# Kernel optimization log

Hardware: AMD Instinct MI355X
Metric: run time of the kernel (lower is better)

The kernel has to match this reference:

```python
import jax, jax.numpy as jnp
import numpy as np

EPS = 1e-06
K = 32


def setup_inputs() -> dict:
    key = jax.random.key(0)
    k1, k2, k3, k4, k5 = jax.random.split(key, 5)
    d_model, n_latents = 1024, 16384
    x = jax.random.normal(k1, (2, 2048, d_model), dtype=jnp.float32)
    b_pre = jax.random.normal(k2, (d_model,), dtype=jnp.float32) * 0.02
    W_enc = jax.random.normal(k3, (n_latents, d_model), dtype=jnp.float32) / np.sqrt(d_model)
    b_enc = jax.random.normal(k4, (n_latents,), dtype=jnp.float32) * 0.02
    W_dec = jax.random.normal(k5, (d_model, n_latents), dtype=jnp.float32)
    # mimic normalize_decoder_weights: unit norm along dim=1 (n_latents axis per row)
    W_dec = W_dec / jnp.linalg.norm(W_dec, axis=1, keepdims=True)
    return {"x": x, "b_pre": b_pre, "W_enc": W_enc, "b_enc": b_enc, "W_dec": W_dec}


def reference(x, b_pre, W_enc, b_enc, W_dec):
    B, S, D = x.shape
    # preprocess: center + normalize (torch .std is unbiased, ddof=1)
    mean = jnp.mean(x, axis=-1, keepdims=True)
    norm = jnp.std(x, axis=-1, keepdims=True, ddof=1) + EPS
    xn = ((x - mean) / norm).reshape(-1, D)          # [N, D]
    # encode
    h = (xn - b_pre) @ W_enc.T + b_enc               # [N, n_latents]
    # top-k + relu + scatter into sparse latent
    vals, idx = jax.lax.top_k(h, K)                  # [N, K]
    vals = jax.nn.relu(vals)
    rows = jnp.arange(h.shape[0])[:, None]
    h_sparse = jnp.zeros_like(h).at[rows, idx].set(vals)
    # decode (dense matmul over mostly-zero latents, as in the original)
    recon = h_sparse @ W_dec.T + b_pre               # [N, D]
    # postprocess: denormalize
    recon = recon.reshape(B, S, D) * norm + mean
    return recon
```

## Files before the change

### kernel.cpp

```cpp
#include <hip/hip_runtime.h>
#include <cstdint>
#include <cstddef>

typedef _Float16 half_t;
typedef _Float16 half4_t __attribute__((ext_vector_type(4)));
typedef _Float16 half8_t __attribute__((ext_vector_type(8)));
typedef unsigned short ushort8_t __attribute__((ext_vector_type(8)));
typedef float floatx4 __attribute__((ext_vector_type(4)));

#define NROWS 4096
#define DMODEL 1024
#define NLAT 16384
#define CAND_MAX 256

#define MBYTE (1ull << 20)
static const size_t oW0    = 0;
static const size_t oWdT   = 32 * MBYTE;
static const size_t oMeanF = 64 * MBYTE;
static const size_t oNormF = 64 * MBYTE + (64ull << 10);
static const size_t oMeanD = 64 * MBYTE + (128ull << 10);
static const size_t oNormD = 64 * MBYTE + (192ull << 10);
static const size_t oCandC = 64 * MBYTE + (256ull << 10);
static const size_t oCandI = 65 * MBYTE;
static const size_t oCandV = 69 * MBYTE;
static const size_t oBatch = 77 * MBYTE;

#define BATCH_ROW_BYTES 34816ull

__device__ __forceinline__ void gload16(const void* g, void* l) {
  __builtin_amdgcn_global_load_lds(
      (const __attribute__((address_space(1))) void*)g,
      (__attribute__((address_space(3))) void*)l, 16, 0, 0);
}

__device__ __forceinline__ uint32_t okey16(uint32_t u) {
  return (u & 0x8000u) ? ((~u) & 0xFFFFu) : (u | 0x8000u);
}
__device__ __forceinline__ float inv_okey16(uint32_t k) {
  unsigned short u = (k & 0x8000u) ? (unsigned short)(k & 0x7FFFu)
                                   : (unsigned short)(~k);
  return (float)__builtin_bit_cast(_Float16, u);
}

#define WSPLIT_B 2048
#define TRANS_B  4096
__global__ __launch_bounds__(256) void prepro_kernel(
    const float* __restrict__ x, const float* __restrict__ b_pre,
    const float* __restrict__ W_enc, const float* __restrict__ Wd,
    half_t* __restrict__ W0h, half_t* __restrict__ WdT,
    half_t* __restrict__ X0,
    float* __restrict__ meanF, float* __restrict__ normF,
    double* __restrict__ meanD, double* __restrict__ normD, int r0) {
  int bid = blockIdx.x, tid = threadIdx.x;
  if (bid < WSPLIT_B) {
    size_t base = (size_t)bid * 2048 + tid;
    for (int it = 0; it < 8; ++it) {
      size_t i = base + (size_t)it * 256;
      float4 v = ((const float4*)W_enc)[i];
      half4_t h0;
      h0[0] = (half_t)(v.x * 1024.0f);
      h0[1] = (half_t)(v.y * 1024.0f);
      h0[2] = (half_t)(v.z * 1024.0f);
      h0[3] = (half_t)(v.w * 1024.0f);
      ((half4_t*)W0h)[i] = h0;
    }
    return;
  }
  if (bid < WSPLIT_B + TRANS_B) {
    __shared__ float tile[64][65];
    int t = bid - WSPLIT_B;
    int c0 = (t & 255) * 64;
    int r0t = (t >> 8) * 64;
    int tc = tid & 63, tg = tid >> 6;
    for (int i = 0; i < 16; ++i) {
      int rr = i * 4 + tg;
      tile[rr][tc] = Wd[(size_t)(r0t + rr) * NLAT + c0 + tc];
    }
    __syncthreads();
    for (int i = 0; i < 16; ++i) {
      int cc = i * 4 + tg;
      WdT[(size_t)(c0 + cc) * DMODEL + r0t + tc] = (half_t)tile[tc][cc];
    }
    return;
  }
  int rl = bid - WSPLIT_B - TRANS_B;
  int rg = r0 + rl;
  const float4* px = (const float4*)(x + (size_t)rg * DMODEL);
  float4 v = px[tid];
  double s  = (double)v.x + (double)v.y + (double)v.z + (double)v.w;
  double sq = (double)v.x * v.x + (double)v.y * v.y +
              (double)v.z * v.z + (double)v.w * v.w;
  for (int off = 32; off; off >>= 1) {
    s += __shfl_down(s, off);
    sq += __shfl_down(sq, off);
  }
  __shared__ double ss[4], ssq[4];
  __shared__ double sMean, sNorm;
  int wv = tid >> 6, ln = tid & 63;
  if (ln == 0) { ss[wv] = s; ssq[wv] = sq; }
  __syncthreads();
  if (tid == 0) {
    double S = ss[0] + ss[1] + ss[2] + ss[3];
    double Q = ssq[0] + ssq[1] + ssq[2] + ssq[3];
    double mean = S / (double)DMODEL;
    double var = (Q - (double)DMODEL * mean * mean) / (double)(DMODEL - 1);
    double nrm = sqrt(var) + 1e-6;
    sMean = mean; sNorm = nrm;
    meanF[rg] = (float)mean; normF[rg] = (float)nrm;
    meanD[rg] = mean;        normD[rg] = nrm;
  }
  __syncthreads();
  float mean = (float)sMean, nrm = (float)sNorm;
  const float4* pb = (const float4*)b_pre;
  float4 bp = pb[tid];
  float c[4];
  c[0] = ((v.x - mean) / nrm - bp.x) * 1024.0f;
  c[1] = ((v.y - mean) / nrm - bp.y) * 1024.0f;
  c[2] = ((v.z - mean) / nrm - bp.z) * 1024.0f;
  c[3] = ((v.w - mean) / nrm - bp.w) * 1024.0f;
  half4_t h0;
  for (int i = 0; i < 4; ++i) h0[i] = (half_t)c[i];
  ((half4_t*)(X0 + (size_t)rl * DMODEL))[tid] = h0;
}

__global__ __launch_bounds__(512, 2) void gemm_enc(
    const half_t* __restrict__ X0, const half_t* __restrict__ W0,
    const float* __restrict__ b_enc, half_t* __restrict__ h, int mtiles) {
  __shared__ __align__(16) half_t As[2][256 * 64];
  __shared__ __align__(16) half_t Bs[2][256 * 64];
  int tid = threadIdx.x;
  int lane = tid & 63, wave = tid >> 6;
  int wm = wave >> 2, wn = wave & 3;

  int bid = blockIdx.x;
  int xcd = bid & 7, q = bid >> 3;
  int bn = xcd * 8 + (q & 7);
  int bm = q >> 3;
  (void)mtiles;

  const char* Ag = (const char*)(X0 + (size_t)bm * 256 * DMODEL);
  const char* Bg = (const char*)(W0 + (size_t)bn * 256 * DMODEL);

  int srcSwz = ((lane & 7) ^ (lane >> 3)) << 4;
  int rowBase = wave * 8 + (lane >> 3);
  int ldsWOff = wave * 1024;

#define STAGE(b, kt)                                                          \
  {                                                                           \
    int colB = (kt) * 128 + srcSwz;                                           \
    _Pragma("unroll") for (int i = 0; i < 4; ++i) {                           \
      size_t go = (size_t)(i * 64 + rowBase) * 2048 + colB;                   \
      gload16(Ag + go, (char*)As[b] + i * 8192 + ldsWOff);                    \
      gload16(Bg + go, (char*)Bs[b] + i * 8192 + ldsWOff);                    \
    }                                                                         \
  }

  floatx4 acc[8][4] = {};

  STAGE(0, 0);
  STAGE(1, 1);
  asm volatile("s_waitcnt vmcnt(8)" ::: "memory");
  __builtin_amdgcn_sched_barrier(0);
  __builtin_amdgcn_s_barrier();
  __builtin_amdgcn_sched_barrier(0);

  int laneQ = (lane & 15) * 128 + (lane >> 4) * 16;
  int sxor = (lane & 7) << 4;
  int aRow = wm * 128 * 128;
  int bRow = wn * 64 * 128;

  for (int kt = 0; kt < 16; ++kt) {
    int cur = kt & 1;
    const char* Ab = (const char*)As[cur];
    const char* Bb = (const char*)Bs[cur];
    for (int kk = 0; kk < 2; ++kk) {
      int kOff = kk * 64 + laneQ;
      half8_t a[8], b[4];
#pragma unroll
      for (int mi = 0; mi < 8; ++mi)
        a[mi] = *(const half8_t*)(Ab + ((aRow + mi * 2048 + kOff) ^ sxor));
#pragma unroll
      for (int ni = 0; ni < 4; ++ni)
        b[ni] = *(const half8_t*)(Bb + ((bRow + ni * 2048 + kOff) ^ sxor));
      __builtin_amdgcn_s_setprio(1);
#pragma unroll
      for (int mi = 0; mi < 8; ++mi)
#pragma unroll
        for (int ni = 0; ni < 4; ++ni)
          acc[mi][ni] = __builtin_amdgcn_mfma_f32_16x16x32_f16(
              a[mi], b[ni], acc[mi][ni], 0, 0, 0);
      __builtin_amdgcn_s_setprio(0);
    }
    if (kt == 15) break;
    __builtin_amdgcn_s_barrier();
    if (kt + 2 < 16) {
      STAGE(cur, kt + 2);
      asm volatile("s_waitcnt vmcnt(8)" ::: "memory");
    } else {
      asm volatile("s_waitcnt vmcnt(0)" ::: "memory");
    }
    __builtin_amdgcn_sched_barrier(0);
    __builtin_amdgcn_s_barrier();
    __builtin_amdgcn_sched_barrier(0);
  }
#undef STAGE

  const float scale = 0x1p-20f;
  int rowb = bm * 256 + wm * 128 + ((lane >> 4) * 4);
  int colb = bn * 256 + wn * 64 + (lane & 15);
  float be[4];
#pragma unroll
  for (int ni = 0; ni < 4; ++ni) be[ni] = b_enc[colb + ni * 16];
#pragma unroll
  for (int mi = 0; mi < 8; ++mi)
#pragma unroll
    for (int ni = 0; ni < 4; ++ni)
#pragma unroll
      for (int r = 0; r < 4; ++r)
        h[(size_t)(rowb + mi * 16 + r) * NLAT + colb + ni * 16] =
            (half_t)(acc[mi][ni][r] * scale + be[ni]);
}

__global__ __launch_bounds__(256) void cand_kernel(
    const half_t* __restrict__ h, int* __restrict__ candIdx,
    int* __restrict__ candCnt, int r0) {
  int rl = blockIdx.x, tid = threadIdx.x;
  int rg = r0 + rl;
  const ushort8_t* ph8 = (const ushort8_t*)(h + (size_t)rl * NLAT);
  __shared__ uint32_t hist[8192];
  __shared__ int chunkSum[256];
  __shared__ float sThresh;
  __shared__ int cCount;

  for (int i = tid; i < 8192; i += 256) hist[i] = 0;
  if (tid == 0) cCount = 0;
  __syncthreads();

  for (int i = 0; i < 8; ++i) {
    ushort8_t v = ph8[tid + i * 256];
#pragma unroll
    for (int e = 0; e < 8; ++e)
      atomicAdd(&hist[okey16((uint32_t)v[e]) >> 3], 1u);
  }
  __syncthreads();
  {
    int s = 0;
    for (int b = 0; b < 32; ++b) s += (int)hist[tid * 32 + b];
    chunkSum[tid] = s;
  }
  __syncthreads();
  if (tid == 0) {
    int cum = 0, cchunk = 255;
    for (; cchunk > 0; --cchunk) {
      if (cum + chunkSum[cchunk] >= 32) break;
      cum += chunkSum[cchunk];
    }
    int b = cchunk * 32 + 31;
    for (; b > 0; --b) {
      if (cum + (int)hist[b] >= 32) break;
      cum += (int)hist[b];
    }
    sThresh = inv_okey16((uint32_t)b << 3) - 0.02f;
  }
  __syncthreads();
  float thresh = sThresh;

  for (int i = 0; i < 8; ++i) {
    ushort8_t v = ph8[tid + i * 256];
#pragma unroll
    for (int e = 0; e < 8; ++e) {
      float f = (float)__builtin_bit_cast(_Float16, (unsigned short)v[e]);
      if (f >= thresh) {
        int j = (tid + i * 256) * 8 + e;
        int slot = atomicAdd(&cCount, 1);
        if (slot < CAND_MAX) candIdx[(size_t)rg * CAND_MAX + slot] = j;
      }
    }
  }
  __syncthreads();
  if (tid == 0) candCnt[rg] = (cCount < CAND_MAX) ? cCount : CAND_MAX;
}

__global__ __launch_bounds__(256) void refine_dot(
    const float* __restrict__ x, const float* __restrict__ b_pre,
    const float* __restrict__ W_enc, const float* __restrict__ b_enc,
    const double* __restrict__ meanD, const double* __restrict__ normD,
    const int* __restrict__ candIdx, const int* __restrict__ candCnt,
    double* __restrict__ candV, int r0) {
  int rg = r0 + blockIdx.x;
  int tid = threadIdx.x;
  int wv = tid >> 6, ln = tid & 63;
  double mean = meanD[rg], nrm = normD[rg];
  const float* px = x + (size_t)rg * DMODEL;
  double xr[16];
#pragma unroll
  for (int u = 0; u < 16; ++u)
    xr[u] = ((double)px[ln + u * 64] - mean) / nrm - (double)b_pre[ln + u * 64];
  int nc = candCnt[rg];
  const int* ci = candIdx + (size_t)rg * CAND_MAX;

  for (int c0 = wv * 4; c0 < nc; c0 += 16) {
    const float* wp[4];
#pragma unroll
    for (int q = 0; q < 4; ++q) {
      int c = c0 + q;
      int j = ci[c < nc ? c : (nc - 1)];
      wp[q] = W_enc + (size_t)j * DMODEL + ln;
    }
    double a0 = 0.0, a1 = 0.0, a2 = 0.0, a3 = 0.0;
#pragma unroll
    for (int u = 0; u < 16; ++u) {
      float w0 = wp[0][u * 64];
      float w1 = wp[1][u * 64];
      float w2 = wp[2][u * 64];
      float w3 = wp[3][u * 64];
      a0 += xr[u] * (double)w0;
      a1 += xr[u] * (double)w1;
      a2 += xr[u] * (double)w2;
      a3 += xr[u] * (double)w3;
    }
    double accq[4] = {a0, a1, a2, a3};
#pragma unroll
    for (int q = 0; q < 4; ++q) {
      double s = accq[q];
      for (int off = 32; off; off >>= 1) s += __shfl_down(s, off);
      int c = c0 + q;
      if (ln == 0 && c < nc) {
        int j = ci[c];
        candV[(size_t)rg * CAND_MAX + c] = s + (double)b_enc[j];
      }
    }
  }
}

__global__ __launch_bounds__(256) void sel_decode(
    const double* __restrict__ candV, const int* __restrict__ candIdx,
    const int* __restrict__ candCnt,
    const half_t* __restrict__ WdT, const float* __restrict__ b_pre,
    const float* __restrict__ meanF, const float* __restrict__ normF,
    float* __restrict__ out, int r0) {
  int rg = r0 + blockIdx.x, tid = threadIdx.x;
  __shared__ double cV[CAND_MAX];
  __shared__ int cI[CAND_MAX];
  __shared__ float sVal[32];
  __shared__ int sIdx[32];
  int nc = candCnt[rg];
  for (int c = tid; c < nc; c += 256) {
    cV[c] = candV[(size_t)rg * CAND_MAX + c];
    cI[c] = candIdx[(size_t)rg * CAND_MAX + c];
  }
  if (tid < 32) { sVal[tid] = 0.0f; sIdx[tid] = 0; }
  __syncthreads();
  for (int c = tid; c < nc; c += 256) {
    double v = cV[c];
    int ix = cI[c];
    int rank = 0;
    for (int o = 0; o < nc; ++o) {
      double vo = cV[o];
      int io = cI[o];
      rank += (vo > v || (vo == v && io < ix)) ? 1 : 0;
    }
    if (rank < 32) {
      sIdx[rank] = ix;
      sVal[rank] = (float)(v > 0.0 ? v : 0.0);
    }
  }
  __syncthreads();
  int d0 = tid * 4;
  float4 accv = {0.f, 0.f, 0.f, 0.f};
#pragma unroll 8
  for (int k = 0; k < 32; ++k) {
    float vk = sVal[k];
    const half4_t wv = *(const half4_t*)(WdT + (size_t)sIdx[k] * DMODEL + d0);
    accv.x += vk * (float)wv[0]; accv.y += vk * (float)wv[1];
    accv.z += vk * (float)wv[2]; accv.w += vk * (float)wv[3];
  }
  float4 bp = ((const float4*)b_pre)[tid];
  float nrm = normF[rg], mn = meanF[rg];
  float4 o;
  o.x = (accv.x + bp.x) * nrm + mn;
  o.y = (accv.y + bp.y) * nrm + mn;
  o.z = (accv.z + bp.z) * nrm + mn;
  o.w = (accv.w + bp.w) * nrm + mn;
  ((float4*)(out + (size_t)rg * DMODEL))[tid] = o;
}

extern "C" void kernel_launch(void* const* d_in, const int* in_sizes, int n_in,
                              void* d_out, int out_size, void* d_ws, size_t ws_size,
                              hipStream_t stream) {
  const float* x     = (const float*)d_in[0];
  const float* b_pre = (const float*)d_in[1];
  const float* W_enc = (const float*)d_in[2];
  const float* b_enc = (const float*)d_in[3];
  const float* W_dec = (const float*)d_in[4];
  float* out = (float*)d_out;
  char* ws = (char*)d_ws;

  int rowsB = NROWS;
  while (rowsB > 256) {
    size_t need = oBatch + (size_t)rowsB * BATCH_ROW_BYTES;
    if (need <= ws_size) break;
    rowsB >>= 1;
  }
  if (oBatch + (size_t)rowsB * BATCH_ROW_BYTES > ws_size) return;

  half_t* W0 = (half_t*)(ws + oW0);
  half_t* WdT = (half_t*)(ws + oWdT);
  float* meanF = (float*)(ws + oMeanF);
  float* normF = (float*)(ws + oNormF);
  double* meanD = (double*)(ws + oMeanD);
  double* normD = (double*)(ws + oNormD);
  int*   candCnt = (int*)(ws + oCandC);
  int*   candIdx = (int*)(ws + oCandI);
  double* candV  = (double*)(ws + oCandV);
  half_t* X0b  = (half_t*)(ws + oBatch);
  half_t* hb   = X0b + (size_t)rowsB * DMODEL;

  for (int r0 = 0; r0 < NROWS; r0 += rowsB) {
    hipLaunchKernelGGL(prepro_kernel,
                       dim3(WSPLIT_B + TRANS_B + rowsB), dim3(256), 0, stream,
                       x, b_pre, W_enc, W_dec, W0, WdT, X0b,
                       meanF, normF, meanD, normD, r0);
    int mtiles = rowsB / 256;
    hipLaunchKernelGGL(gemm_enc, dim3(mtiles * 64), dim3(512), 0, stream,
                       X0b, W0, b_enc, hb, mtiles);
    hipLaunchKernelGGL(cand_kernel, dim3(rowsB), dim3(256), 0, stream,
                       hb, candIdx, candCnt, r0);
    hipLaunchKernelGGL(refine_dot, dim3(rowsB), dim3(256), 0, stream,
                       x, b_pre, W_enc, b_enc, meanD, normD, candIdx, candCnt,
                       candV, r0);
    hipLaunchKernelGGL(sel_decode, dim3(rowsB), dim3(256), 0, stream,
                       candV, candIdx, candCnt, WdT, b_pre, meanF, normF, out, r0);
  }
}
```

Before: 378.2 us.

## Interleave staged global loads with MFMA phases in encoder GEMM main loop

Restructures the encoder GEMM K-loop into an 8-phase schedule per pair of tiles. Each phase issues half-tile global-to-LDS loads between fragment reads and MFMA bursts, with barriers and lgkm/vmcnt waits placed explicitly. The goal is to spread memory traffic across compute so load latency hides better than with the old bulk stage-then-compute loop. In exchange there are many more barriers per tile. Loads wrap past the last tile (kt&15), so the final iterations issue redundant loads.

New measurement: 372.7 us. Within noise of the previous version (-1.4%).

```diff
diff --git a/kernel.cpp b/kernel.cpp
--- a/kernel.cpp
+++ b/kernel.cpp
@@ -145,65 +145,93 @@
   int rowBase = wave * 8 + (lane >> 3);
   int ldsWOff = wave * 1024;
 
-#define STAGE(b, kt)                                                          \
-  {                                                                           \
-    int colB = (kt) * 128 + srcSwz;                                           \
-    _Pragma("unroll") for (int i = 0; i < 4; ++i) {                           \
-      size_t go = (size_t)(i * 64 + rowBase) * 2048 + colB;                   \
-      gload16(Ag + go, (char*)As[b] + i * 8192 + ldsWOff);                    \
-      gload16(Bg + go, (char*)Bs[b] + i * 8192 + ldsWOff);                    \
-    }                                                                         \
-  }
+#define STG_A(b, kt, pr) { int colB = ((kt) & 15) * 128 + srcSwz;             \
+    gload16(Ag + (size_t)((pr) * 64 + rowBase) * 2048 + colB,                 \
+            (char*)As[b] + (pr) * 8192 + ldsWOff);                            \
+    gload16(Ag + (size_t)(((pr) + 2) * 64 + rowBase) * 2048 + colB,           \
+            (char*)As[b] + ((pr) + 2) * 8192 + ldsWOff); }
+#define STG_B(b, kt, pr) { int colB = ((kt) & 15) * 128 + srcSwz;             \
+    gload16(Bg + (size_t)((pr) * 64 + rowBase) * 2048 + colB,                 \
+            (char*)Bs[b] + (pr) * 8192 + ldsWOff);                            \
+    gload16(Bg + (size_t)(((pr) + 2) * 64 + rowBase) * 2048 + colB,           \
+            (char*)Bs[b] + ((pr) + 2) * 8192 + ldsWOff); }
 
   floatx4 acc[8][4] = {};
 
-  STAGE(0, 0);
-  STAGE(1, 1);
-  asm volatile("s_waitcnt vmcnt(8)" ::: "memory");
+  STG_B(0, 0, 0); STG_B(0, 0, 1); STG_A(0, 0, 0); STG_A(0, 0, 1);
+  STG_B(1, 1, 0); STG_B(1, 1, 1); STG_A(1, 1, 0);
+  asm volatile("s_waitcnt vmcnt(6)" ::: "memory");
   __builtin_amdgcn_sched_barrier(0);
   __builtin_amdgcn_s_barrier();
-  __builtin_amdgcn_sched_barrier(0);
 
   int laneQ = (lane & 15) * 128 + (lane >> 4) * 16;
   int sxor = (lane & 7) << 4;
   int aRow = wm * 128 * 128;
   int bRow = wn * 64 * 128;
 
-  for (int kt = 0; kt < 16; ++kt) {
-    int cur = kt & 1;
-    const char* Ab = (const char*)As[cur];
-    const char* Bb = (const char*)Bs[cur];
-    for (int kk = 0; kk < 2; ++kk) {
-      int kOff = kk * 64 + laneQ;
-      half8_t a[8], b[4];
-#pragma unroll
-      for (int mi = 0; mi < 8; ++mi)
-        a[mi] = *(const half8_t*)(Ab + ((aRow + mi * 2048 + kOff) ^ sxor));
-#pragma unroll
-      for (int ni = 0; ni < 4; ++ni)
-        b[ni] = *(const half8_t*)(Bb + ((bRow + ni * 2048 + kOff) ^ sxor));
-      __builtin_amdgcn_s_setprio(1);
-#pragma unroll
-      for (int mi = 0; mi < 8; ++mi)
-#pragma unroll
-        for (int ni = 0; ni < 4; ++ni)
-          acc[mi][ni] = __builtin_amdgcn_mfma_f32_16x16x32_f16(
-              a[mi], b[ni], acc[mi][ni], 0, 0, 0);
-      __builtin_amdgcn_s_setprio(0);
-    }
-    if (kt == 15) break;
-    __builtin_amdgcn_s_barrier();
-    if (kt + 2 < 16) {
-      STAGE(cur, kt + 2);
-      asm volatile("s_waitcnt vmcnt(8)" ::: "memory");
-    } else {
-      asm volatile("s_waitcnt vmcnt(0)" ::: "memory");
-    }
-    __builtin_amdgcn_sched_barrier(0);
-    __builtin_amdgcn_s_barrier();
-    __builtin_amdgcn_sched_barrier(0);
-  }
-#undef STAGE
+  half8_t bfr[2][4], afr[4];
+  const char *Ab, *Bb;
+
+#define LD_A(mh, kk) _Pragma("unroll") for (int t = 0; t < 4; ++t)            \
+    afr[t] = *(const half8_t*)(Ab + ((aRow + ((mh) * 4 + t) * 2048 +          \
+                                      (kk) * 64 + laneQ) ^ sxor));
+#define LD_B(kk) _Pragma("unroll") for (int t = 0; t < 4; ++t)                \
+    bfr[kk][t] = *(const half8_t*)(Bb + ((bRow + t * 2048 +                   \
+                                          (kk) * 64 + laneQ) ^ sxor));
+#define MM(mb, kk) __builtin_amdgcn_s_setprio(1);                             \
+    _Pragma("unroll") for (int mi = 0; mi < 4; ++mi)                          \
+    _Pragma("unroll") for (int ni = 0; ni < 4; ++ni)                          \
+      acc[(mb) + mi][ni] = __builtin_amdgcn_mfma_f32_16x16x32_f16(            \
+          afr[mi], bfr[kk][ni], acc[(mb) + mi][ni], 0, 0, 0);                 \
+    __builtin_amdgcn_s_setprio(0);
+#define BAR() __builtin_amdgcn_s_barrier()
+#define LGKM0() { asm volatile("s_waitcnt lgkmcnt(0)" ::: "memory");          \
+    __builtin_amdgcn_sched_barrier(0); }
+#define VM6() { asm volatile("s_waitcnt vmcnt(6)" ::: "memory");              \
+    __builtin_amdgcn_sched_barrier(0); }
+
+#pragma unroll 1
+  for (int i = 0; i < 8; ++i) {
+    int t0 = 2 * i;
+    Ab = (const char*)As[0]; Bb = (const char*)Bs[0];
+    LD_B(0); LD_B(1); LD_A(0, 0);
+    STG_A(1, t0 + 1, 1);
+    BAR(); LGKM0(); MM(0, 0); BAR();
+    LD_A(1, 0);
+    STG_B(0, t0 + 2, 0);
+    BAR(); LGKM0(); MM(4, 0); BAR();
+    LD_A(0, 1);
+    STG_B(0, t0 + 2, 1);
+    BAR(); LGKM0(); MM(0, 1); BAR();
+    LD_A(1, 1);
+    STG_A(0, t0 + 2, 0);
+    BAR(); LGKM0(); MM(4, 1);
+    VM6();
+    BAR();
+    Ab = (const char*)As[1]; Bb = (const char*)Bs[1];
+    LD_B(0); LD_B(1); LD_A(0, 0);
+    STG_A(0, t0 + 2, 1);
+    BAR(); LGKM0(); MM(0, 0); BAR();
+    LD_A(1, 0);
+    STG_B(1, t0 + 3, 0);
+    BAR(); LGKM0(); MM(4, 0); BAR();
+    LD_A(0, 1);
+    STG_B(1, t0 + 3, 1);
+    BAR(); LGKM0(); MM(0, 1); BAR();
+    LD_A(1, 1);
+    STG_A(1, t0 + 3, 0);
+    BAR(); LGKM0(); MM(4, 1);
+    VM6();
+    BAR();
+  }
+#undef STG_A
+#undef STG_B
+#undef LD_A
+#undef LD_B
+#undef MM
+#undef BAR
+#undef LGKM0
+#undef VM6
 
   const float scale = 0x1p-20f;
   int rowb = bm * 256 + wm * 128 + ((lane >> 4) * 4);
```
